# Optimization experiments

Measured on AMD Instinct MI355X. Metric: run time of the kernel, lower is better.

## Reference

```python
import jax, jax.numpy as jnp
import numpy as np

B, S, V, E, H, T = 256, 160, 50000, 300, 256, 200

def setup_inputs() -> dict:
    key = jax.random.key(0)
    ks = jax.random.split(key, 12)
    return {
        'x1': jax.random.randint(ks[0], (B, S), 0, V),
        'x2': jax.random.randint(ks[1], (B, S), 0, V),
        'x1mask': jnp.ones((B, S), jnp.float32),
        'key_c': jax.random.normal(ks[2], (B, S, T), jnp.float32) * 0.1,
        'key_r': jax.random.normal(ks[3], (B, S, T), jnp.float32) * 0.1,
        'emb_table': jax.random.normal(ks[4], (V, E), jnp.float32) * 0.1,
        'W_ih': jax.random.normal(ks[5], (4 * H, E), jnp.float32) * 0.05,
        'W_hh': jax.random.normal(ks[6], (4 * H, H), jnp.float32) * 0.05,
        'W_kh': jax.random.normal(ks[7], (4 * H, T), jnp.float32) * 0.05,
        'b_g': jnp.zeros((4 * H,), jnp.float32),
        'W_attn': jax.random.normal(ks[8], (H, H), jnp.float32) * 0.05,
        'b_attn': jnp.zeros((H,), jnp.float32),
        'M': jax.random.normal(ks[9], (H, H), jnp.float32) * 0.05,
        'b': jnp.zeros((1,), jnp.float32),
    }

def _run_rnn(x_emb, k_emb, W_ih, W_hh, W_kh, b_g):
    # x_emb: [B,S,E], k_emb: [B,S,T] -> hidden states [B,S,H]
    Bn = x_emb.shape[0]
    h0 = jnp.zeros((Bn, H), x_emb.dtype)
    c0 = jnp.zeros((Bn, H), x_emb.dtype)
    def cell(carry, inp):
        h, c = carry
        x_t, k_t = inp
        g = x_t @ W_ih.T + h @ W_hh.T + k_t @ W_kh.T + b_g  # [B,4H]
        i, f, gg, o = jnp.split(g, 4, axis=-1)
        c = jax.nn.sigmoid(f) * c + jax.nn.sigmoid(i) * jnp.tanh(gg)
        h = jax.nn.sigmoid(o) * jnp.tanh(c)
        return (h, c), h
    xs = (jnp.swapaxes(x_emb, 0, 1), jnp.swapaxes(k_emb, 0, 1))  # time-major
    (_, _), hs = jax.lax.scan(cell, (h0, c0), xs)
    return jnp.swapaxes(hs, 0, 1)  # [B,S,H]

def reference(x1, x2, x1mask, key_c, key_r, emb_table, W_ih, W_hh, W_kh, b_g,
              W_attn, b_attn, M, b):
    x1_emb = emb_table[x1]  # [B,S,E] (dropout = identity at eval)
    x2_emb = emb_table[x2]
    sc = _run_rnn(x1_emb, key_c, W_ih, W_hh, W_kh, b_g)  # context states [B,S,H]
    rs = _run_rnn(x2_emb, key_r, W_ih, W_hh, W_kh, b_g)
    r = rs[:, -1]  # last response hidden [B,H]
    # masked dot-product attention over context states keyed by r
    attn = sc @ W_attn.T + b_attn  # [B,S,H]
    energies = jnp.einsum('bsh,bh->bs', attn, r) * x1mask
    alpha = jax.nn.softmax(energies, axis=-1)
    c_attn = jnp.einsum('bs,bsh->bh', alpha, sc)
    # bilinear score
    o = jnp.einsum('bh,hk,bk->b', c_attn, M, r) + b[0]
    return o
```

## Files before the change

kernel.cpp:

```cpp
#include <hip/hip_runtime.h>
#include <math.h>

#define B_   256
#define S_   160
#define E_   300
#define H_   256
#define T_   200
#define G4H  1024
#define CH   16
#define NCH  10

typedef float  f32x4  __attribute__((ext_vector_type(4)));
typedef __bf16 bf16x4 __attribute__((ext_vector_type(4)));
typedef __bf16 bf16x8 __attribute__((ext_vector_type(8)));

__device__ __forceinline__ float sigf(float x) {
    float e = expf(-fabsf(x));
    float p = 1.0f / (1.0f + e);
    return x >= 0.0f ? p : e * p;
}

__device__ __forceinline__ int norig(int np) {
    return ((np >> 4) & 3) * 256 + ((np >> 6) << 4) + (np & 15);
}

__device__ __forceinline__ float4 pick4(const float* __restrict__ e,
                                        const float* __restrict__ k, int kg) {
    if (kg < E_)      return *(const float4*)(e + kg);
    if (kg < E_ + T_) return *(const float4*)(k + (kg - E_));
    return make_float4(0.f, 0.f, 0.f, 0.f);
}

__device__ __forceinline__ void split4(float4 v, bf16x4& h, bf16x4& l) {
    h[0] = (__bf16)v.x; l[0] = (__bf16)(v.x - (float)h[0]);
    h[1] = (__bf16)v.y; l[1] = (__bf16)(v.y - (float)h[1]);
    h[2] = (__bf16)v.z; l[2] = (__bf16)(v.z - (float)h[2]);
    h[3] = (__bf16)v.w; l[3] = (__bf16)(v.w - (float)h[3]);
}

__global__ __launch_bounds__(128) void prep_split(
    const float* __restrict__ Whh, const float* __restrict__ Wih,
    const float* __restrict__ Wkh,
    __bf16* __restrict__ whh_hi, __bf16* __restrict__ whh_lo,
    __bf16* __restrict__ wik_hi, __bf16* __restrict__ wik_lo)
{
    const int n  = blockIdx.x;
    const int np = ((n & 255) >> 4) * 64 + (n >> 8) * 16 + (n & 15);
    const int t  = threadIdx.x;
    {
        const int k4 = t * 4;
        float4 v;
        if (k4 < E_)            v = *(const float4*)(Wih + (size_t)n * E_ + k4);
        else if (k4 < E_ + T_)  v = *(const float4*)(Wkh + (size_t)n * T_ + (k4 - E_));
        else                    v = make_float4(0.f, 0.f, 0.f, 0.f);
        bf16x4 h, l;
        split4(v, h, l);
        *(bf16x4*)(wik_hi + (size_t)np * 512 + k4) = h;
        *(bf16x4*)(wik_lo + (size_t)np * 512 + k4) = l;
    }
    if (t < 64) {
        const int k4 = t * 4;
        const float4 v = *(const float4*)(Whh + (size_t)n * 256 + k4);
        bf16x4 h, l;
        split4(v, h, l);
        *(bf16x4*)(whh_hi + (size_t)np * 256 + k4) = h;
        *(bf16x4*)(whh_lo + (size_t)np * 256 + k4) = l;
    }
}

__global__ __launch_bounds__(512, 2) void gemm_g2(
    const int* __restrict__ x1, const int* __restrict__ x2,
    const float* __restrict__ key_c, const float* __restrict__ key_r,
    const float* __restrict__ emb,
    const __bf16* __restrict__ wik_hi, const __bf16* __restrict__ wik_lo,
    const float* __restrict__ bg,
    float* __restrict__ G, int s0)
{
    __shared__ __align__(16) __bf16 Ah[128 * 32];
    __shared__ __align__(16) __bf16 Al[128 * 32];
    __shared__ __align__(16) __bf16 Bh[128 * 32];
    __shared__ __align__(16) __bf16 Bl[128 * 32];

    const int t   = threadIdx.x;
    const int rnn = blockIdx.z;
    const int m0  = blockIdx.x * 128;
    const int n0  = blockIdx.y * 128;
    const int* xx = rnn ? x2 : x1;
    const float* key = rnn ? key_r : key_c;

    const int r0 = t >> 2;
    const int cq = t & 3;
    const int csw = ((cq ^ ((r0 >> 1) & 3)) * 16);

    const float* aeb; const float* akb;
    const __bf16* wph; const __bf16* wpl;
    {
        const int am = m0 + r0;
        const int bs = (am >> 4) * S_ + s0 + (am & 15);
        aeb = emb + (size_t)xx[bs] * E_;
        akb = key + (size_t)bs * T_;
        wph = wik_hi + (size_t)(n0 + r0) * 512;
        wpl = wik_lo + (size_t)(n0 + r0) * 512;
    }

    const int w  = t >> 6;
    const int wm = w >> 2;
    const int wn = w & 3;
    const int l  = t & 63;
    const int cl = l & 15;
    const int ch = l >> 4;
    const int chs = ((ch ^ ((cl >> 1) & 3)) * 16);

    f32x4 acc[4][2];
    #pragma unroll
    for (int fm = 0; fm < 4; ++fm)
        #pragma unroll
        for (int fn = 0; fn < 2; ++fn) acc[fm][fn] = (f32x4){0.f, 0.f, 0.f, 0.f};

    float4 va0 = pick4(aeb, akb, cq * 8);
    float4 va1 = pick4(aeb, akb, cq * 8 + 4);
    bf16x8 vbh = *(const bf16x8*)(wph + cq * 8);
    bf16x8 vbl = *(const bf16x8*)(wpl + cq * 8);

    for (int kt = 0; kt < 16; ++kt) {
        bf16x4 h0, l0, h1, l1;
        split4(va0, h0, l0);
        split4(va1, h1, l1);
        const bf16x8 sah = __builtin_shufflevector(h0, h1, 0, 1, 2, 3, 4, 5, 6, 7);
        const bf16x8 sal = __builtin_shufflevector(l0, l1, 0, 1, 2, 3, 4, 5, 6, 7);
        const bf16x8 sbh = vbh;
        const bf16x8 sbl = vbl;
        __syncthreads();
        {
            const int off = r0 * 64 + csw;
            *(bf16x8*)((char*)Ah + off) = sah;
            *(bf16x8*)((char*)Al + off) = sal;
            *(bf16x8*)((char*)Bh + off) = sbh;
            *(bf16x8*)((char*)Bl + off) = sbl;
        }
        __syncthreads();

        if (kt < 15) {
            const int kg = (kt + 1) * 32 + cq * 8;
            va0 = pick4(aeb, akb, kg);
            va1 = pick4(aeb, akb, kg + 4);
            vbh = *(const bf16x8*)(wph + kg);
            vbl = *(const bf16x8*)(wpl + kg);
        }

        bf16x8 fBh[2], fBl[2];
        #pragma unroll
        for (int fn = 0; fn < 2; ++fn) {
            const int off = (wn * 32 + fn * 16 + cl) * 64 + chs;
            fBh[fn] = *(const bf16x8*)((const char*)Bh + off);
            fBl[fn] = *(const bf16x8*)((const char*)Bl + off);
        }
        #pragma unroll
        for (int fm = 0; fm < 4; ++fm) {
            const int off = (wm * 64 + fm * 16 + cl) * 64 + chs;
            const bf16x8 fAh = *(const bf16x8*)((const char*)Ah + off);
            const bf16x8 fAl = *(const bf16x8*)((const char*)Al + off);
            #pragma unroll
            for (int fn = 0; fn < 2; ++fn) {
                acc[fm][fn] = __builtin_amdgcn_mfma_f32_16x16x32_bf16(fAh, fBh[fn], acc[fm][fn], 0, 0, 0);
                acc[fm][fn] = __builtin_amdgcn_mfma_f32_16x16x32_bf16(fAh, fBl[fn], acc[fm][fn], 0, 0, 0);
                acc[fm][fn] = __builtin_amdgcn_mfma_f32_16x16x32_bf16(fAl, fBh[fn], acc[fm][fn], 0, 0, 0);
            }
        }
    }

    float bgl[2];
    #pragma unroll
    for (int fn = 0; fn < 2; ++fn)
        bgl[fn] = bg[norig(n0 + wn * 32 + fn * 16 + cl)];

    #pragma unroll
    for (int fm = 0; fm < 4; ++fm) {
        #pragma unroll
        for (int r = 0; r < 4; ++r) {
            const int m  = m0 + wm * 64 + fm * 16 + ch * 4 + r;
            const int b  = m >> 4;
            const int sl = m & 15;
            float* rowp = G + ((size_t)(rnn * CH + sl) * B_ + b) * G4H;
            #pragma unroll
            for (int fn = 0; fn < 2; ++fn)
                rowp[n0 + wn * 32 + fn * 16 + cl] = acc[fm][fn][r] + bgl[fn];
        }
    }
}

__global__ __launch_bounds__(256, 2) void lstm_ks(
    const float* __restrict__ G,
    const __bf16* __restrict__ Whi, const __bf16* __restrict__ Wlo,
    const __bf16* __restrict__ hhi_in, const __bf16* __restrict__ hlo_in,
    __bf16* __restrict__ hhi_out, __bf16* __restrict__ hlo_out,
    float* __restrict__ cst, float* __restrict__ sc,
    int sl, int s_glob, int first)
{
    __shared__ float ps[64 * 66];

    const int t  = threadIdx.x;
    const int w  = t >> 6;
    const int l  = t & 63;
    const int cl = l & 15;
    const int ch = l >> 4;
    const int mt = blockIdx.x;
    const int jt = blockIdx.y;
    const int rnn = mt >> 4;
    const int b0  = (mt & 15) * 16;
    const int m0  = mt * 16;

    const int me = t >> 4;
    const int jl = t & 15;
    const int j  = jt * 16 + jl;
    float Ge[4];
    const float* Gb = G + ((size_t)(rnn * CH + sl) * B_ + b0 + me) * G4H + jt * 64;
    #pragma unroll
    for (int g = 0; g < 4; ++g) Ge[g] = Gb[g * 16 + jl];
    const float c_in = first ? 0.f : cst[(size_t)(m0 + me) * 256 + j];

    const size_t ab = (size_t)(m0 + cl) * 256 + w * 64 + ch * 8;
    const bf16x8 fAh0 = *(const bf16x8*)(hhi_in + ab);
    const bf16x8 fAh1 = *(const bf16x8*)(hhi_in + ab + 32);
    const bf16x8 fAl0 = *(const bf16x8*)(hlo_in + ab);
    const bf16x8 fAl1 = *(const bf16x8*)(hlo_in + ab + 32);

    bf16x8 fBh[4][2], fBl[4][2];
    #pragma unroll
    for (int g = 0; g < 4; ++g) {
        const size_t bb = (size_t)(jt * 64 + g * 16 + cl) * 256 + w * 64 + ch * 8;
        fBh[g][0] = *(const bf16x8*)(Whi + bb);
        fBh[g][1] = *(const bf16x8*)(Whi + bb + 32);
        fBl[g][0] = *(const bf16x8*)(Wlo + bb);
        fBl[g][1] = *(const bf16x8*)(Wlo + bb + 32);
    }

    f32x4 acc[4];
    #pragma unroll
    for (int g = 0; g < 4; ++g) acc[g] = (f32x4){0.f, 0.f, 0.f, 0.f};
    #pragma unroll
    for (int g = 0; g < 4; ++g) {
        acc[g] = __builtin_amdgcn_mfma_f32_16x16x32_bf16(fAh0, fBh[g][0], acc[g], 0, 0, 0);
        acc[g] = __builtin_amdgcn_mfma_f32_16x16x32_bf16(fAh1, fBh[g][1], acc[g], 0, 0, 0);
        acc[g] = __builtin_amdgcn_mfma_f32_16x16x32_bf16(fAh0, fBl[g][0], acc[g], 0, 0, 0);
        acc[g] = __builtin_amdgcn_mfma_f32_16x16x32_bf16(fAh1, fBl[g][1], acc[g], 0, 0, 0);
        acc[g] = __builtin_amdgcn_mfma_f32_16x16x32_bf16(fAl0, fBh[g][0], acc[g], 0, 0, 0);
        acc[g] = __builtin_amdgcn_mfma_f32_16x16x32_bf16(fAl1, fBh[g][1], acc[g], 0, 0, 0);
    }

    #pragma unroll
    for (int g = 0; g < 4; ++g)
        #pragma unroll
        for (int r = 0; r < 4; ++r)
            ps[(w * 16 + ch * 4 + r) * 66 + g * 16 + cl] = acc[g][r];
    __syncthreads();

    float g4[4];
    #pragma unroll
    for (int g = 0; g < 4; ++g) {
        float s = Ge[g];
        #pragma unroll
        for (int w2 = 0; w2 < 4; ++w2)
            s += ps[(w2 * 16 + me) * 66 + g * 16 + jl];
        g4[g] = s;
    }
    const float c = sigf(g4[1]) * c_in + sigf(g4[0]) * tanhf(g4[2]);
    const float h = sigf(g4[3]) * tanhf(c);
    cst[(size_t)(m0 + me) * 256 + j] = c;
    const __bf16 hh = (__bf16)h;
    const size_t ho = (size_t)(m0 + me) * 256 + j;
    hhi_out[ho] = hh;
    hlo_out[ho] = (__bf16)(h - (float)hh);
    if (rnn == 0)
        sc[((size_t)(b0 + me) * S_ + s_glob) * H_ + j] = h;
}

__global__ __launch_bounds__(256) void final_kernel(
    const float* __restrict__ sc,
    const __bf16* __restrict__ rhi, const __bf16* __restrict__ rlo,
    const float* __restrict__ Wattn, const float* __restrict__ battn,
    const float* __restrict__ M, const float* __restrict__ bscal,
    const float* __restrict__ mask, float* __restrict__ out)
{
    __shared__ float rs[256], us[256], red[256], as_[256];
    const int b = blockIdx.x;
    const int t = threadIdx.x;

    const size_t ri = (size_t)(256 + b) * 256 + t;
    rs[t] = (float)rhi[ri] + (float)rlo[ri];
    __syncthreads();

    float acc = 0.0f;
    for (int h = 0; h < 256; ++h) acc += rs[h] * Wattn[h * 256 + t];
    us[t] = acc;

    red[t] = battn[t] * rs[t];
    __syncthreads();
    for (int off = 128; off; off >>= 1) {
        if (t < off) red[t] += red[t + off];
        __syncthreads();
    }
    float beta = red[0];
    __syncthreads();

    float vh = 0.0f;
    {
        const float* Mrow = M + t * 256;
        for (int k = 0; k < 256; ++k) vh += Mrow[k] * rs[k];
    }

    float e = -INFINITY;
    if (t < S_) {
        float d = 0.0f;
        const float* scrow = sc + ((size_t)b * S_ + t) * H_;
        for (int h = 0; h < 256; ++h) d += scrow[h] * us[h];
        e = (d + beta) * mask[b * S_ + t];
    }
    red[t] = e;
    __syncthreads();
    for (int off = 128; off; off >>= 1) {
        if (t < off) red[t] = fmaxf(red[t], red[t + off]);
        __syncthreads();
    }
    float mx = red[0];
    __syncthreads();

    float p = (t < S_) ? expf(e - mx) : 0.0f;
    as_[t] = p;
    red[t] = p;
    __syncthreads();
    for (int off = 128; off; off >>= 1) {
        if (t < off) red[t] += red[t + off];
        __syncthreads();
    }
    float inv = 1.0f / red[0];
    __syncthreads();

    float ca = 0.0f;
    for (int s = 0; s < S_; ++s) ca += as_[s] * sc[((size_t)b * S_ + s) * H_ + t];
    ca *= inv;

    red[t] = ca * vh;
    __syncthreads();
    for (int off = 128; off; off >>= 1) {
        if (t < off) red[t] += red[t + off];
        __syncthreads();
    }
    if (t == 0) out[b] = red[0] + bscal[0];
}

extern "C" void kernel_launch(void* const* d_in, const int* in_sizes, int n_in,
                              void* d_out, int out_size, void* d_ws, size_t ws_size,
                              hipStream_t stream)
{
    const int*   x1    = (const int*)d_in[0];
    const int*   x2    = (const int*)d_in[1];
    const float* mask  = (const float*)d_in[2];
    const float* key_c = (const float*)d_in[3];
    const float* key_r = (const float*)d_in[4];
    const float* emb   = (const float*)d_in[5];
    const float* Wih   = (const float*)d_in[6];
    const float* Whh   = (const float*)d_in[7];
    const float* Wkh   = (const float*)d_in[8];
    const float* bg    = (const float*)d_in[9];
    const float* Wattn = (const float*)d_in[10];
    const float* battn = (const float*)d_in[11];
    const float* M     = (const float*)d_in[12];
    const float* bb    = (const float*)d_in[13];
    float* out = (float*)d_out;
    char*  wsb = (char*)d_ws;

    float*  G     = (float*)(wsb + 0);
    float*  sc    = (float*)(wsb + 33554432);
    __bf16* hhi0  = (__bf16*)(wsb + 75497472);
    __bf16* hlo0  = (__bf16*)(wsb + 75759616);
    __bf16* hhi1  = (__bf16*)(wsb + 76021760);
    __bf16* hlo1  = (__bf16*)(wsb + 76283904);
    float*  cst   = (float*)(wsb + 76546048);
    __bf16* WhhHi = (__bf16*)(wsb + 77070336);
    __bf16* WhhLo = (__bf16*)(wsb + 77594624);
    __bf16* WikHi = (__bf16*)(wsb + 78118912);
    __bf16* WikLo = (__bf16*)(wsb + 79167488);
    if (ws_size < 80216064) return;

    hipMemsetAsync(hhi0, 0, 524288, stream);
    prep_split<<<dim3(1024), 128, 0, stream>>>(Whh, Wih, Wkh,
                                               WhhHi, WhhLo, WikHi, WikLo);

    for (int ci = 0; ci < NCH; ++ci) {
        gemm_g2<<<dim3(32, 8, 2), 512, 0, stream>>>(x1, x2, key_c, key_r, emb,
                                                    WikHi, WikLo, bg, G, ci * CH);
        for (int slq = 0; slq < CH; ++slq) {
            const int s   = ci * CH + slq;
            const int par = s & 1;
            lstm_ks<<<dim3(32, 16), 256, 0, stream>>>(G, WhhHi, WhhLo,
                                                      par ? hhi1 : hhi0,
                                                      par ? hlo1 : hlo0,
                                                      par ? hhi0 : hhi1,
                                                      par ? hlo0 : hlo1,
                                                      cst, sc, slq, s, s == 0);
        }
    }

    final_kernel<<<dim3(256), 256, 0, stream>>>(sc, hhi0, hlo0, Wattn, battn,
                                                M, bb, mask, out);
}
```

Before: 1.485 ms.

## Double gemm block to 1024 threads with half staging, add fast tanh

The input-projection GEMM now launches 1024 threads per block. Only the first 512 threads stage the A/B tiles into LDS, and each of the 16 waves computes a 32x32 sub-tile instead of 64x32, which halves accumulators per thread and raises the wave count so MFMA and LDS latency can be hidden. The LSTM cell also replaces tanhf with a sigmoid-based tanh to reduce transcendental cost. The tanh form can lose a little precision near zero, and the launch bound of 1024 with 8 blocks per CU may force register spilling.

```diff
diff --git a/kernel.cpp b/kernel.cpp
--- a/kernel.cpp
+++ b/kernel.cpp
@@ -18,6 +18,10 @@
     float e = expf(-fabsf(x));
     float p = 1.0f / (1.0f + e);
     return x >= 0.0f ? p : e * p;
+}
+
+__device__ __forceinline__ float tanhf_fast(float x) {
+    return 2.0f * sigf(2.0f * x) - 1.0f;
 }
 
 __device__ __forceinline__ int norig(int np) {
@@ -68,7 +72,7 @@
     }
 }
 
-__global__ __launch_bounds__(512, 2) void gemm_g2(
+__global__ __launch_bounds__(1024, 8) void gemm_g2(
     const int* __restrict__ x1, const int* __restrict__ x2,
     const float* __restrict__ key_c, const float* __restrict__ key_r,
     const float* __restrict__ emb,
@@ -88,13 +92,14 @@
     const int* xx = rnn ? x2 : x1;
     const float* key = rnn ? key_r : key_c;
 
-    const int r0 = t >> 2;
+    const bool stager = (t < 512);
+    const int r0 = (t & 511) >> 2;
     const int cq = t & 3;
     const int csw = ((cq ^ ((r0 >> 1) & 3)) * 16);
 
-    const float* aeb; const float* akb;
-    const __bf16* wph; const __bf16* wpl;
-    {
+    const float* aeb = emb; const float* akb = key_c;
+    const __bf16* wph = wik_hi; const __bf16* wpl = wik_lo;
+    if (stager) {
         const int am = m0 + r0;
         const int bs = (am >> 4) * S_ + s0 + (am & 15);
         aeb = emb + (size_t)xx[bs] * E_;
@@ -111,27 +116,36 @@
     const int ch = l >> 4;
     const int chs = ((ch ^ ((cl >> 1) & 3)) * 16);
 
-    f32x4 acc[4][2];
-    #pragma unroll
-    for (int fm = 0; fm < 4; ++fm)
+    f32x4 acc[2][2];
+    #pragma unroll
+    for (int fm = 0; fm < 2; ++fm)
         #pragma unroll
         for (int fn = 0; fn < 2; ++fn) acc[fm][fn] = (f32x4){0.f, 0.f, 0.f, 0.f};
 
-    float4 va0 = pick4(aeb, akb, cq * 8);
-    float4 va1 = pick4(aeb, akb, cq * 8 + 4);
-    bf16x8 vbh = *(const bf16x8*)(wph + cq * 8);
-    bf16x8 vbl = *(const bf16x8*)(wpl + cq * 8);
+    float4 va0 = make_float4(0.f, 0.f, 0.f, 0.f);
+    float4 va1 = va0;
+    bf16x8 vbh = {};
+    bf16x8 vbl = {};
+    if (stager) {
+        va0 = pick4(aeb, akb, cq * 8);
+        va1 = pick4(aeb, akb, cq * 8 + 4);
+        vbh = *(const bf16x8*)(wph + cq * 8);
+        vbl = *(const bf16x8*)(wpl + cq * 8);
+    }
 
     for (int kt = 0; kt < 16; ++kt) {
-        bf16x4 h0, l0, h1, l1;
-        split4(va0, h0, l0);
-        split4(va1, h1, l1);
-        const bf16x8 sah = __builtin_shufflevector(h0, h1, 0, 1, 2, 3, 4, 5, 6, 7);
-        const bf16x8 sal = __builtin_shufflevector(l0, l1, 0, 1, 2, 3, 4, 5, 6, 7);
-        const bf16x8 sbh = vbh;
-        const bf16x8 sbl = vbl;
-        __syncthreads();
-        {
+        bf16x8 sah, sal, sbh, sbl;
+        if (stager) {
+            bf16x4 h0, l0, h1, l1;
+            split4(va0, h0, l0);
+            split4(va1, h1, l1);
+            sah = __builtin_shufflevector(h0, h1, 0, 1, 2, 3, 4, 5, 6, 7);
+            sal = __builtin_shufflevector(l0, l1, 0, 1, 2, 3, 4, 5, 6, 7);
+            sbh = vbh;
+            sbl = vbl;
+        }
+        __syncthreads();
+        if (stager) {
             const int off = r0 * 64 + csw;
             *(bf16x8*)((char*)Ah + off) = sah;
             *(bf16x8*)((char*)Al + off) = sal;
@@ -140,7 +154,7 @@
         }
         __syncthreads();
 
-        if (kt < 15) {
+        if (stager && kt < 15) {
             const int kg = (kt + 1) * 32 + cq * 8;
             va0 = pick4(aeb, akb, kg);
             va1 = pick4(aeb, akb, kg + 4);
@@ -156,8 +170,8 @@
             fBl[fn] = *(const bf16x8*)((const char*)Bl + off);
         }
         #pragma unroll
-        for (int fm = 0; fm < 4; ++fm) {
-            const int off = (wm * 64 + fm * 16 + cl) * 64 + chs;
+        for (int fm = 0; fm < 2; ++fm) {
+            const int off = (wm * 32 + fm * 16 + cl) * 64 + chs;
             const bf16x8 fAh = *(const bf16x8*)((const char*)Ah + off);
             const bf16x8 fAl = *(const bf16x8*)((const char*)Al + off);
             #pragma unroll
@@ -175,10 +189,10 @@
         bgl[fn] = bg[norig(n0 + wn * 32 + fn * 16 + cl)];
 
     #pragma unroll
-    for (int fm = 0; fm < 4; ++fm) {
+    for (int fm = 0; fm < 2; ++fm) {
         #pragma unroll
         for (int r = 0; r < 4; ++r) {
-            const int m  = m0 + wm * 64 + fm * 16 + ch * 4 + r;
+            const int m  = m0 + wm * 32 + fm * 16 + ch * 4 + r;
             const int b  = m >> 4;
             const int sl = m & 15;
             float* rowp = G + ((size_t)(rnn * CH + sl) * B_ + b) * G4H;
@@ -264,8 +278,8 @@
             s += ps[(w2 * 16 + me) * 66 + g * 16 + jl];
         g4[g] = s;
     }
-    const float c = sigf(g4[1]) * c_in + sigf(g4[0]) * tanhf(g4[2]);
-    const float h = sigf(g4[3]) * tanhf(c);
+    const float c = sigf(g4[1]) * c_in + sigf(g4[0]) * tanhf_fast(g4[2]);
+    const float h = sigf(g4[3]) * tanhf_fast(c);
     cst[(size_t)(m0 + me) * 256 + j] = c;
     const __bf16 hh = (__bf16)h;
     const size_t ho = (size_t)(m0 + me) * 256 + j;
@@ -388,8 +402,8 @@
                                                WhhHi, WhhLo, WikHi, WikLo);
 
     for (int ci = 0; ci < NCH; ++ci) {
-        gemm_g2<<<dim3(32, 8, 2), 512, 0, stream>>>(x1, x2, key_c, key_r, emb,
-                                                    WikHi, WikLo, bg, G, ci * CH);
+        gemm_g2<<<dim3(32, 8, 2), 1024, 0, stream>>>(x1, x2, key_c, key_r, emb,
+                                                     WikHi, WikLo, bg, G, ci * CH);
         for (int slq = 0; slq < CH; ++slq) {
             const int s   = ci * CH + slq;
             const int par = s & 1;
```

New measurement: 2.358 ms. 1.59x slower.
